# Optimization experiments

Hardware: AMD Instinct MI355X
Metric: run time of the kernel (lower is better)

Reference implementation:

```python
import math
import jax, jax.numpy as jnp
import numpy as np
from jax import lax

L = 16
T = 256
FDIM = 3
N_MIN = 4
N_MAX = 64
INIT_RANGE = 1e-4
# low 32 bits of the products are exact in uint32, and XOR + (% T) with T=256
# only reads the low 8 bits, so uint32 arithmetic matches torch's int64 exactly.
PI = jnp.array([1, 2654435761, 805459861], dtype=jnp.uint32)

def _levels():
    growth = math.exp(math.log(N_MAX / N_MIN) / (L - 1))
    return [math.floor(N_MIN * growth ** l) for l in range(L)]

def setup_inputs() -> dict:
    key = jax.random.key(0)
    kx, kt = jax.random.split(key)
    x = jax.random.uniform(kx, (4, 3, 64, 64, 64), dtype=jnp.float32)
    hash_table = (jax.random.uniform(kt, (L, T, FDIM), dtype=jnp.float32) * 2.0
                  - 1.0) * INIT_RANGE
    return {"x": x, "hash_table": hash_table}

def _forward(x, hash_table):
    b, c, h, w, d = x.shape
    outs = []
    for l, n in enumerate(_levels()):
        kh, kw, kd = h // n, w // n, d // n
        # max_pool3d with kernel==stride, VALID padding (torch default)
        pooled = lax.reduce_window(x * n, -jnp.inf, lax.max,
                                   (1, 1, kh, kw, kd), (1, 1, kh, kw, kd),
                                   'VALID')  # [b, 3, nh, nw, nd]
        g = pooled.astype(jnp.uint32)  # trunc toward zero (values >= 0)
        g = g * PI.reshape(1, 3, 1, 1, 1)
        gh = (g[:, 0] ^ g[:, 1] ^ g[:, 2]) % jnp.uint32(T)  # [b, nh, nw, nd]
        feat = hash_table[l][gh]                 # [b, nh, nw, nd, F] gather
        feat = jnp.transpose(feat, (0, 4, 1, 3, 2))  # [b, F, nh, nd, nw]
        up = jax.image.resize(feat, (b, FDIM, h, w, d), method='trilinear')
        outs.append(up)
    return jnp.concatenate(outs, axis=1)  # [b, L*F, h, w, d]

def reference(x, hash_table):
    return _forward(x, hash_table)
```

## Files before the change

kernel.cpp:

```cpp
#include <hip/hip_runtime.h>
#include <cmath>
#include <cstdint>
#include <cstddef>

using u32 = unsigned int;
typedef float f32x4 __attribute__((ext_vector_type(4)));

__device__ inline void nt_store4(float* p, float a, float b, float c, float d)
{
    f32x4 v; v.x = a; v.y = b; v.z = c; v.w = d;
    __builtin_nontemporal_store(v, (f32x4*)p);
}

constexpr int NH[12] = {4,4,5,6,8,10,12,16,21,21,32,32};

constexpr int OFF_M2  = 0;
constexpr int OFF_M3  = 393216;
constexpr int OFF_M5  = 504348;
constexpr int OFF_M4  = 525084;
constexpr int OFF_M6  = 574236;
constexpr int OFF_M8  = 586236;
constexpr int OFF_M10 = 592380;
constexpr int OFF_M12 = 594972;
constexpr int OFF_M16 = 596472;

constexpr int POFF[12] = {OFF_M16,OFF_M16,OFF_M12,OFF_M10,OFF_M8,OFF_M6,
                          OFF_M5, OFF_M4, OFF_M3, OFF_M3, OFF_M2, OFF_M2};

constexpr float invf_of(int nh){ return (float)(1.0/(64.0/(double)nh)); }
constexpr float INVF[12] = {invf_of(4),invf_of(4),invf_of(5),invf_of(6),
                            invf_of(8),invf_of(10),invf_of(12),invf_of(16),
                            invf_of(21),invf_of(21),invf_of(32),invf_of(32)};

struct HP { int n[16]; };

__device__ inline float lp(float a, float b, float w){ return fmaf(w, b - a, a); }

__global__ __launch_bounds__(256) void k_pool_base(const float* __restrict__ x,
                                                   float* __restrict__ ws)
{
    int tid = blockIdx.x * 256 + threadIdx.x;
    if (tid < 393216) {
        int pd = tid & 31, pw = (tid >> 5) & 31, ph = (tid >> 10) & 31;
        int bc = tid >> 15;
        const float* xp = x + (size_t)bc * 262144 + (ph*2)*4096 + (pw*2)*64 + pd*2;
        float2 v00 = *(const float2*)(xp);
        float2 v01 = *(const float2*)(xp + 64);
        float2 v10 = *(const float2*)(xp + 4096);
        float2 v11 = *(const float2*)(xp + 4160);
        float m = fmaxf(fmaxf(fmaxf(v00.x,v00.y), fmaxf(v01.x,v01.y)),
                        fmaxf(fmaxf(v10.x,v10.y), fmaxf(v11.x,v11.y)));
        ws[OFF_M2 + tid] = m;
    } else if (tid < 504348) {
        int idx = tid - 393216;
        int pd = idx % 21; int t2 = idx / 21;
        int pw = t2 % 21;  int t3 = t2 / 21;
        int ph = t3 % 21;  int bc = t3 / 21;
        const float* xp = x + (size_t)bc * 262144 + (ph*3)*4096 + (pw*3)*64 + pd*3;
        float m = -1.f;
        #pragma unroll
        for (int dh = 0; dh < 3; ++dh)
        #pragma unroll
        for (int dw = 0; dw < 3; ++dw) {
            const float* r = xp + dh*4096 + dw*64;
            m = fmaxf(m, fmaxf(fmaxf(r[0], r[1]), r[2]));
        }
        ws[OFF_M3 + idx] = m;
    } else if (tid < 525084) {
        int idx = tid - 504348;
        int pd = idx % 12; int t2 = idx / 12;
        int pw = t2 % 12;  int t3 = t2 / 12;
        int ph = t3 % 12;  int bc = t3 / 12;
        const float* xp = x + (size_t)bc * 262144 + (ph*5)*4096 + (pw*5)*64 + pd*5;
        float m = -1.f;
        #pragma unroll
        for (int dh = 0; dh < 5; ++dh)
        #pragma unroll
        for (int dw = 0; dw < 5; ++dw) {
            const float* r = xp + dh*4096 + dw*64;
            m = fmaxf(m, fmaxf(fmaxf(fmaxf(r[0],r[1]), fmaxf(r[2],r[3])), r[4]));
        }
        ws[OFF_M5 + idx] = m;
    }
}

__global__ __launch_bounds__(256) void k_pyr(float* __restrict__ ws)
{
    int tid = blockIdx.x * 256 + threadIdx.x;
    if (tid < 49152) {
        int w = tid >> 6, lane = tid & 63;
        int pd = w & 3, pw = (w >> 2) & 3, ph = (w >> 4) & 3, bc = w >> 6;
        const float* m2 = ws + OFF_M2 + (size_t)bc*32768 + (ph*8)*1024 + (pw*8)*32 + pd*8;
        float m = -1.f;
        #pragma unroll
        for (int e = 0; e < 8; ++e) {
            int id2 = (e << 6) | lane;
            int dd = id2 & 7, dw = (id2 >> 3) & 7, dh = id2 >> 6;
            m = fmaxf(m, m2[dh*1024 + dw*32 + dd]);
        }
        #pragma unroll
        for (int s = 32; s; s >>= 1) m = fmaxf(m, __shfl_xor(m, s, 64));
        if (lane == 0) ws[OFF_M16 + w] = m;
    } else if (tid < 98304) {
        int idx = tid - 49152;
        int pd = idx & 15, pw = (idx >> 4) & 15, ph = (idx >> 8) & 15, bc = idx >> 12;
        const float* m2 = ws + OFF_M2 + (size_t)bc*32768 + (ph*2)*1024 + (pw*2)*32 + pd*2;
        float2 u0 = *(const float2*)(m2);
        float2 u1 = *(const float2*)(m2 + 32);
        float2 u2 = *(const float2*)(m2 + 1024);
        float2 u3 = *(const float2*)(m2 + 1056);
        ws[OFF_M4 + idx] = fmaxf(fmaxf(fmaxf(u0.x,u0.y), fmaxf(u1.x,u1.y)),
                                 fmaxf(fmaxf(u2.x,u2.y), fmaxf(u3.x,u3.y)));
    } else if (tid < 110304) {
        int idx = tid - 98304;
        int pd = idx % 10; int t2 = idx / 10;
        int pw = t2 % 10;  int t3 = t2 / 10;
        int ph = t3 % 10;  int bc = t3 / 10;
        const float* m2 = ws + OFF_M2 + (size_t)bc*32768 + (ph*3)*1024 + (pw*3)*32 + pd*3;
        float m = -1.f;
        #pragma unroll
        for (int dh = 0; dh < 3; ++dh)
        #pragma unroll
        for (int dw = 0; dw < 3; ++dw) {
            const float* r = m2 + dh*1024 + dw*32;
            m = fmaxf(m, fmaxf(fmaxf(r[0], r[1]), r[2]));
        }
        ws[OFF_M6 + idx] = m;
    } else if (tid < 116448) {
        int idx = tid - 110304;
        int pd = idx & 7, pw = (idx >> 3) & 7, ph = (idx >> 6) & 7, bc = idx >> 9;
        const float* m2 = ws + OFF_M2 + (size_t)bc*32768 + (ph*4)*1024 + (pw*4)*32 + pd*4;
        float m = -1.f;
        #pragma unroll
        for (int dh = 0; dh < 4; ++dh)
        #pragma unroll
        for (int dw = 0; dw < 4; ++dw) {
            float4 v = *(const float4*)(m2 + dh*1024 + dw*32);
            m = fmaxf(m, fmaxf(fmaxf(v.x,v.y), fmaxf(v.z,v.w)));
        }
        ws[OFF_M8 + idx] = m;
    } else if (tid < 119040) {
        int idx = tid - 116448;
        int pd = idx % 6; int t2 = idx / 6;
        int pw = t2 % 6;  int t3 = t2 / 6;
        int ph = t3 % 6;  int bc = t3 / 6;
        const float* m2 = ws + OFF_M2 + (size_t)bc*32768 + (ph*5)*1024 + (pw*5)*32 + pd*5;
        float m = -1.f;
        #pragma unroll
        for (int dh = 0; dh < 5; ++dh)
        #pragma unroll
        for (int dw = 0; dw < 5; ++dw) {
            const float* r = m2 + dh*1024 + dw*32;
            m = fmaxf(m, fmaxf(fmaxf(fmaxf(r[0],r[1]), fmaxf(r[2],r[3])), r[4]));
        }
        ws[OFF_M10 + idx] = m;
    } else if (tid < 120540) {
        int idx = tid - 119040;
        int pd = idx % 5; int t2 = idx / 5;
        int pw = t2 % 5;  int t3 = t2 / 5;
        int ph = t3 % 5;  int bc = t3 / 5;
        const float* m3 = ws + OFF_M3 + (size_t)bc*9261 + (ph*4)*441 + (pw*4)*21 + pd*4;
        float m = -1.f;
        #pragma unroll
        for (int dh = 0; dh < 4; ++dh)
        #pragma unroll
        for (int dw = 0; dw < 4; ++dw) {
            const float* r = m3 + dh*441 + dw*21;
            m = fmaxf(m, fmaxf(fmaxf(r[0],r[1]), fmaxf(r[2],r[3])));
        }
        ws[OFF_M12 + idx] = m;
    }
}

__global__ __launch_bounds__(256) void k_identity(const float* __restrict__ x,
                                                  const float* __restrict__ tbl,
                                                  float* __restrict__ out, HP hp)
{
    __shared__ float  xs[3 * 2112];
    __shared__ float4 tab[1024];
    const int t = threadIdx.x;
    const int b = blockIdx.x >> 7;
    const int i = (blockIdx.x >> 1) & 63;
    const int jh = blockIdx.x & 1;

    for (int v = t; v < 1024; v += 256) {
        const float* te = tbl + (size_t)(3072 + v) * 3;
        tab[v] = make_float4(te[0], te[1], te[2], 0.f);
    }
    const float* xp = x + (size_t)b * 786432 + (size_t)i * 4096 + jh * 32;
    #pragma unroll
    for (int c = 0; c < 3; ++c)
        for (int k = t; k < 2048; k += 256) {
            int w = k >> 5, jl = k & 31;
            xs[c * 2112 + w * 33 + jl] = xp[(size_t)c * 262144 + w * 64 + jl];
        }
    __syncthreads();

    float nfs[4] = {(float)hp.n[12], (float)hp.n[13],
                    (float)hp.n[14], (float)hp.n[15]};
    float* op = out + (size_t)b * 12582912 + (size_t)36 * 262144
                    + (size_t)i * 4096 + jh * 2048;

    #pragma unroll
    for (int it = 0; it < 2; ++it) {
        int pos = it * 256 + t;
        int jl = pos >> 4, d0 = (pos & 15) << 2;
        float xv[3][4];
        #pragma unroll
        for (int dd = 0; dd < 4; ++dd) {
            int wrow = (d0 + dd) * 33 + jl;
            xv[0][dd] = xs[wrow];
            xv[1][dd] = xs[2112 + wrow];
            xv[2][dd] = xs[4224 + wrow];
        }
        #pragma unroll
        for (int u = 0; u < 4; ++u) {
            float4 f[4];
            #pragma unroll
            for (int dd = 0; dd < 4; ++dd) {
                u32 g0 = (u32)(xv[0][dd] * nfs[u]);
                u32 g1 = ((u32)(xv[1][dd] * nfs[u])) * 2654435761u;
                u32 g2 = ((u32)(xv[2][dd] * nfs[u])) * 805459861u;
                f[dd] = tab[(u << 8) | ((g0 ^ g1 ^ g2) & 255u)];
            }
            int off = u * 786432 + jl * 64 + d0;
            nt_store4(op + off,          f[0].x, f[1].x, f[2].x, f[3].x);
            nt_store4(op + off + 262144, f[0].y, f[1].y, f[2].y, f[3].y);
            nt_store4(op + off + 524288, f[0].z, f[1].z, f[2].z, f[3].z);
        }
    }
}

__global__ __launch_bounds__(256) void k_interp(const float* __restrict__ ws,
                                                const float* __restrict__ tbl,
                                                float* __restrict__ out, HP hp)
{
    __shared__ float4 plane[1056];
    const int t = threadIdx.x;
    const int l = blockIdx.y;
    const int b = blockIdx.x >> 6, i = blockIdx.x & 63;
    const int nh = NH[l];
    const int pitch = nh + 1;
    const float iv = INVF[l];
    const float nf = (float)hp.n[l];

    float fi = (float)i + 0.5f;
    float pp = fminf(fmaxf(fi * iv - 0.5f, 0.f), (float)(nh - 1));
    int p0 = min((int)pp, nh - 2);
    float wp = pp - (float)p0;

    const int nsq = nh * nh, ncb = nsq * nh;
    const float* M   = ws + POFF[l] + (size_t)b * 3 * ncb;
    const float* Mp0 = M + p0 * nsq;
    const float* Mp1 = Mp0 + nsq;
    const float* tl  = tbl + (size_t)l * 768;

    for (int idx = t; idx < nsq; idx += 256) {
        int w = idx / nh, d = idx - w * nh;
        float a0 = Mp0[idx], a1 = Mp0[idx + ncb], a2 = Mp0[idx + 2*ncb];
        u32 h0 = ((u32)(a0*nf) ^ (((u32)(a1*nf))*2654435761u)
                               ^ (((u32)(a2*nf))*805459861u)) & 255u;
        const float* t0 = tl + h0 * 3;
        float b0 = Mp1[idx], b1 = Mp1[idx + ncb], b2 = Mp1[idx + 2*ncb];
        u32 h1 = ((u32)(b0*nf) ^ (((u32)(b1*nf))*2654435761u)
                               ^ (((u32)(b2*nf))*805459861u)) & 255u;
        const float* t1 = tl + h1 * 3;
        plane[d * pitch + w] = make_float4(lp(t0[0], t1[0], wp),
                                           lp(t0[1], t1[1], wp),
                                           lp(t0[2], t1[2], wp), 0.f);
    }
    __syncthreads();

    float* op = out + (size_t)b * 12582912 + (size_t)(3 * l) * 262144 + (size_t)i * 4096;
    #pragma unroll
    for (int it = 0; it < 4; ++it) {
        int pos = it * 256 + t;
        int j = pos >> 4, d0 = (pos & 15) << 2;
        float fj = (float)j + 0.5f;
        float pr = fminf(fmaxf(fj * iv - 0.5f, 0.f), (float)(nh - 1));
        int r0 = min((int)pr, nh - 2);
        float wr = pr - (float)r0;
        const float4* P0 = plane + r0 * pitch;
        const float4* P1 = P0 + pitch;
        float ox[4], oy[4], oz[4];
        #pragma unroll
        for (int dd = 0; dd < 4; ++dd) {
            float fk = (float)(d0 + dd) + 0.5f;
            float pq = fminf(fmaxf(fk * iv - 0.5f, 0.f), (float)(nh - 1));
            int q0 = min((int)pq, nh - 2);
            float wq = pq - (float)q0;
            float4 A = P0[q0], B = P0[q0 + 1];
            float4 C = P1[q0], D = P1[q0 + 1];
            float tx = lp(A.x, B.x, wq), bx = lp(C.x, D.x, wq);
            float ty = lp(A.y, B.y, wq), by = lp(C.y, D.y, wq);
            float tz = lp(A.z, B.z, wq), bz = lp(C.z, D.z, wq);
            ox[dd] = lp(tx, bx, wr);
            oy[dd] = lp(ty, by, wr);
            oz[dd] = lp(tz, bz, wr);
        }
        int off = j * 64 + d0;
        nt_store4(op + off,          ox[0], ox[1], ox[2], ox[3]);
        nt_store4(op + off + 262144, oy[0], oy[1], oy[2], oy[3]);
        nt_store4(op + off + 524288, oz[0], oz[1], oz[2], oz[3]);
    }
}

extern "C" void kernel_launch(void* const* d_in, const int* in_sizes, int n_in,
                              void* d_out, int out_size, void* d_ws, size_t ws_size,
                              hipStream_t stream)
{
    const float* x   = (const float*)d_in[0];
    const float* tbl = (const float*)d_in[1];
    float* out = (float*)d_out;
    float* ws  = (float*)d_ws;

    HP hp;
    double growth = std::exp(std::log(16.0) / 15.0);
    for (int l = 0; l < 16; ++l)
        hp.n[l] = (int)std::floor(4.0 * std::pow(growth, (double)l));

    hipLaunchKernelGGL(k_pool_base, dim3(2052),    dim3(256), 0, stream, x, ws);
    hipLaunchKernelGGL(k_pyr,       dim3(471),     dim3(256), 0, stream, ws);
    hipLaunchKernelGGL(k_identity,  dim3(512),     dim3(256), 0, stream, x, tbl, out, hp);
    hipLaunchKernelGGL(k_interp,    dim3(256, 12), dim3(256), 0, stream, ws, tbl, out, hp);
}
```

Measured before the change: 61.33 us.

## Merge identity and interpolation kernels into one launch, use regular stores

Combines the identity-level kernel (levels 12-15) and the trilinear interpolation kernel (levels 0-11) into a single kernel launched on a 256x14 grid. Blocks branch on blockIdx.y and share one union shared-memory buffer. This removes one launch and the tail gap between the two kernels, letting both kinds of work overlap on the GPU. It also replaces nontemporal stores with plain vector stores, which changes cache behaviour for the large output write. The shared buffer grows to the larger of the two footprints, which may reduce occupancy for the interpolation blocks.

```diff
diff --git a/kernel.cpp b/kernel.cpp
--- a/kernel.cpp
+++ b/kernel.cpp
@@ -6,10 +6,10 @@
 using u32 = unsigned int;
 typedef float f32x4 __attribute__((ext_vector_type(4)));
 
-__device__ inline void nt_store4(float* p, float a, float b, float c, float d)
+__device__ inline void st4(float* p, float a, float b, float c, float d)
 {
     f32x4 v; v.x = a; v.y = b; v.z = c; v.w = d;
-    __builtin_nontemporal_store(v, (f32x4*)p);
+    *(f32x4*)p = v;
 }
 
 constexpr int NH[12] = {4,4,5,6,8,10,12,16,21,21,32,32};
@@ -172,136 +172,134 @@
     }
 }
 
-__global__ __launch_bounds__(256) void k_identity(const float* __restrict__ x,
-                                                  const float* __restrict__ tbl,
-                                                  float* __restrict__ out, HP hp)
-{
-    __shared__ float  xs[3 * 2112];
-    __shared__ float4 tab[1024];
-    const int t = threadIdx.x;
-    const int b = blockIdx.x >> 7;
-    const int i = (blockIdx.x >> 1) & 63;
-    const int jh = blockIdx.x & 1;
-
-    for (int v = t; v < 1024; v += 256) {
-        const float* te = tbl + (size_t)(3072 + v) * 3;
-        tab[v] = make_float4(te[0], te[1], te[2], 0.f);
-    }
-    const float* xp = x + (size_t)b * 786432 + (size_t)i * 4096 + jh * 32;
-    #pragma unroll
-    for (int c = 0; c < 3; ++c)
-        for (int k = t; k < 2048; k += 256) {
-            int w = k >> 5, jl = k & 31;
-            xs[c * 2112 + w * 33 + jl] = xp[(size_t)c * 262144 + w * 64 + jl];
-        }
-    __syncthreads();
-
-    float nfs[4] = {(float)hp.n[12], (float)hp.n[13],
-                    (float)hp.n[14], (float)hp.n[15]};
-    float* op = out + (size_t)b * 12582912 + (size_t)36 * 262144
-                    + (size_t)i * 4096 + jh * 2048;
-
-    #pragma unroll
-    for (int it = 0; it < 2; ++it) {
-        int pos = it * 256 + t;
-        int jl = pos >> 4, d0 = (pos & 15) << 2;
-        float xv[3][4];
-        #pragma unroll
-        for (int dd = 0; dd < 4; ++dd) {
-            int wrow = (d0 + dd) * 33 + jl;
-            xv[0][dd] = xs[wrow];
-            xv[1][dd] = xs[2112 + wrow];
-            xv[2][dd] = xs[4224 + wrow];
-        }
-        #pragma unroll
-        for (int u = 0; u < 4; ++u) {
-            float4 f[4];
-            #pragma unroll
-            for (int dd = 0; dd < 4; ++dd) {
-                u32 g0 = (u32)(xv[0][dd] * nfs[u]);
-                u32 g1 = ((u32)(xv[1][dd] * nfs[u])) * 2654435761u;
-                u32 g2 = ((u32)(xv[2][dd] * nfs[u])) * 805459861u;
-                f[dd] = tab[(u << 8) | ((g0 ^ g1 ^ g2) & 255u)];
-            }
-            int off = u * 786432 + jl * 64 + d0;
-            nt_store4(op + off,          f[0].x, f[1].x, f[2].x, f[3].x);
-            nt_store4(op + off + 262144, f[0].y, f[1].y, f[2].y, f[3].y);
-            nt_store4(op + off + 524288, f[0].z, f[1].z, f[2].z, f[3].z);
-        }
-    }
-}
-
-__global__ __launch_bounds__(256) void k_interp(const float* __restrict__ ws,
-                                                const float* __restrict__ tbl,
-                                                float* __restrict__ out, HP hp)
-{
-    __shared__ float4 plane[1056];
+__global__ __launch_bounds__(256) void k_out(const float* __restrict__ x,
+                                             const float* __restrict__ ws,
+                                             const float* __restrict__ tbl,
+                                             float* __restrict__ out, HP hp)
+{
+    __shared__ float4 shb[2608];
     const int t = threadIdx.x;
     const int l = blockIdx.y;
     const int b = blockIdx.x >> 6, i = blockIdx.x & 63;
-    const int nh = NH[l];
-    const int pitch = nh + 1;
-    const float iv = INVF[l];
-    const float nf = (float)hp.n[l];
-
-    float fi = (float)i + 0.5f;
-    float pp = fminf(fmaxf(fi * iv - 0.5f, 0.f), (float)(nh - 1));
-    int p0 = min((int)pp, nh - 2);
-    float wp = pp - (float)p0;
-
-    const int nsq = nh * nh, ncb = nsq * nh;
-    const float* M   = ws + POFF[l] + (size_t)b * 3 * ncb;
-    const float* Mp0 = M + p0 * nsq;
-    const float* Mp1 = Mp0 + nsq;
-    const float* tl  = tbl + (size_t)l * 768;
-
-    for (int idx = t; idx < nsq; idx += 256) {
-        int w = idx / nh, d = idx - w * nh;
-        float a0 = Mp0[idx], a1 = Mp0[idx + ncb], a2 = Mp0[idx + 2*ncb];
-        u32 h0 = ((u32)(a0*nf) ^ (((u32)(a1*nf))*2654435761u)
-                               ^ (((u32)(a2*nf))*805459861u)) & 255u;
-        const float* t0 = tl + h0 * 3;
-        float b0 = Mp1[idx], b1 = Mp1[idx + ncb], b2 = Mp1[idx + 2*ncb];
-        u32 h1 = ((u32)(b0*nf) ^ (((u32)(b1*nf))*2654435761u)
-                               ^ (((u32)(b2*nf))*805459861u)) & 255u;
-        const float* t1 = tl + h1 * 3;
-        plane[d * pitch + w] = make_float4(lp(t0[0], t1[0], wp),
-                                           lp(t0[1], t1[1], wp),
-                                           lp(t0[2], t1[2], wp), 0.f);
-    }
-    __syncthreads();
-
-    float* op = out + (size_t)b * 12582912 + (size_t)(3 * l) * 262144 + (size_t)i * 4096;
-    #pragma unroll
-    for (int it = 0; it < 4; ++it) {
-        int pos = it * 256 + t;
-        int j = pos >> 4, d0 = (pos & 15) << 2;
-        float fj = (float)j + 0.5f;
-        float pr = fminf(fmaxf(fj * iv - 0.5f, 0.f), (float)(nh - 1));
-        int r0 = min((int)pr, nh - 2);
-        float wr = pr - (float)r0;
-        const float4* P0 = plane + r0 * pitch;
-        const float4* P1 = P0 + pitch;
-        float ox[4], oy[4], oz[4];
-        #pragma unroll
-        for (int dd = 0; dd < 4; ++dd) {
-            float fk = (float)(d0 + dd) + 0.5f;
-            float pq = fminf(fmaxf(fk * iv - 0.5f, 0.f), (float)(nh - 1));
-            int q0 = min((int)pq, nh - 2);
-            float wq = pq - (float)q0;
-            float4 A = P0[q0], B = P0[q0 + 1];
-            float4 C = P1[q0], D = P1[q0 + 1];
-            float tx = lp(A.x, B.x, wq), bx = lp(C.x, D.x, wq);
-            float ty = lp(A.y, B.y, wq), by = lp(C.y, D.y, wq);
-            float tz = lp(A.z, B.z, wq), bz = lp(C.z, D.z, wq);
-            ox[dd] = lp(tx, bx, wr);
-            oy[dd] = lp(ty, by, wr);
-            oz[dd] = lp(tz, bz, wr);
-        }
-        int off = j * 64 + d0;
-        nt_store4(op + off,          ox[0], ox[1], ox[2], ox[3]);
-        nt_store4(op + off + 262144, oy[0], oy[1], oy[2], oy[3]);
-        nt_store4(op + off + 524288, oz[0], oz[1], oz[2], oz[3]);
+
+    if (l < 12) {
+        float4* plane = shb;
+        const int nh = NH[l];
+        const int pitch = nh + 1;
+        const float iv = INVF[l];
+        const float nf = (float)hp.n[l];
+
+        float fi = (float)i + 0.5f;
+        float pp = fminf(fmaxf(fi * iv - 0.5f, 0.f), (float)(nh - 1));
+        int p0 = min((int)pp, nh - 2);
+        float wp = pp - (float)p0;
+
+        const int nsq = nh * nh, ncb = nsq * nh;
+        const float* M   = ws + POFF[l] + (size_t)b * 3 * ncb;
+        const float* Mp0 = M + p0 * nsq;
+        const float* Mp1 = Mp0 + nsq;
+        const float* tl  = tbl + (size_t)l * 768;
+
+        for (int idx = t; idx < nsq; idx += 256) {
+            int w = idx / nh, d = idx - w * nh;
+            float a0 = Mp0[idx], a1 = Mp0[idx + ncb], a2 = Mp0[idx + 2*ncb];
+            u32 h0 = ((u32)(a0*nf) ^ (((u32)(a1*nf))*2654435761u)
+                                   ^ (((u32)(a2*nf))*805459861u)) & 255u;
+            const float* t0 = tl + h0 * 3;
+            float b0 = Mp1[idx], b1 = Mp1[idx + ncb], b2 = Mp1[idx + 2*ncb];
+            u32 h1 = ((u32)(b0*nf) ^ (((u32)(b1*nf))*2654435761u)
+                                   ^ (((u32)(b2*nf))*805459861u)) & 255u;
+            const float* t1 = tl + h1 * 3;
+            plane[d * pitch + w] = make_float4(lp(t0[0], t1[0], wp),
+                                               lp(t0[1], t1[1], wp),
+                                               lp(t0[2], t1[2], wp), 0.f);
+        }
+        __syncthreads();
+
+        float* op = out + (size_t)b * 12582912 + (size_t)(3 * l) * 262144
+                        + (size_t)i * 4096;
+        #pragma unroll
+        for (int it = 0; it < 4; ++it) {
+            int pos = it * 256 + t;
+            int j = pos >> 4, d0 = (pos & 15) << 2;
+            float fj = (float)j + 0.5f;
+            float pr = fminf(fmaxf(fj * iv - 0.5f, 0.f), (float)(nh - 1));
+            int r0 = min((int)pr, nh - 2);
+            float wr = pr - (float)r0;
+            const float4* P0 = plane + r0 * pitch;
+            const float4* P1 = P0 + pitch;
+            float ox[4], oy[4], oz[4];
+            #pragma unroll
+            for (int dd = 0; dd < 4; ++dd) {
+                float fk = (float)(d0 + dd) + 0.5f;
+                float pq = fminf(fmaxf(fk * iv - 0.5f, 0.f), (float)(nh - 1));
+                int q0 = min((int)pq, nh - 2);
+                float wq = pq - (float)q0;
+                float4 A = P0[q0], B = P0[q0 + 1];
+                float4 C = P1[q0], D = P1[q0 + 1];
+                float tx = lp(A.x, B.x, wq), bx = lp(C.x, D.x, wq);
+                float ty = lp(A.y, B.y, wq), by = lp(C.y, D.y, wq);
+                float tz = lp(A.z, B.z, wq), bz = lp(C.z, D.z, wq);
+                ox[dd] = lp(tx, bx, wr);
+                oy[dd] = lp(ty, by, wr);
+                oz[dd] = lp(tz, bz, wr);
+            }
+            int off = j * 64 + d0;
+            st4(op + off,          ox[0], ox[1], ox[2], ox[3]);
+            st4(op + off + 262144, oy[0], oy[1], oy[2], oy[3]);
+            st4(op + off + 524288, oz[0], oz[1], oz[2], oz[3]);
+        }
+    } else {
+        float4* tab = shb;
+        float*  xs  = (float*)(shb + 1024);
+        const int jh = l - 12;
+
+        for (int v = t; v < 1024; v += 256) {
+            const float* te = tbl + (size_t)(3072 + v) * 3;
+            tab[v] = make_float4(te[0], te[1], te[2], 0.f);
+        }
+        const float* xp = x + (size_t)b * 786432 + (size_t)i * 4096 + jh * 32;
+        #pragma unroll
+        for (int c = 0; c < 3; ++c)
+            for (int k = t; k < 2048; k += 256) {
+                int w = k >> 5, jl = k & 31;
+                xs[c * 2112 + w * 33 + jl] = xp[(size_t)c * 262144 + w * 64 + jl];
+            }
+        __syncthreads();
+
+        float nfs[4] = {(float)hp.n[12], (float)hp.n[13],
+                        (float)hp.n[14], (float)hp.n[15]};
+        float* op = out + (size_t)b * 12582912 + (size_t)36 * 262144
+                        + (size_t)i * 4096 + jh * 2048;
+
+        #pragma unroll
+        for (int it = 0; it < 2; ++it) {
+            int pos = it * 256 + t;
+            int jl = pos >> 4, d0 = (pos & 15) << 2;
+            float xv[3][4];
+            #pragma unroll
+            for (int dd = 0; dd < 4; ++dd) {
+                int wrow = (d0 + dd) * 33 + jl;
+                xv[0][dd] = xs[wrow];
+                xv[1][dd] = xs[2112 + wrow];
+                xv[2][dd] = xs[4224 + wrow];
+            }
+            #pragma unroll
+            for (int u = 0; u < 4; ++u) {
+                float4 f[4];
+                #pragma unroll
+                for (int dd = 0; dd < 4; ++dd) {
+                    u32 g0 = (u32)(xv[0][dd] * nfs[u]);
+                    u32 g1 = ((u32)(xv[1][dd] * nfs[u])) * 2654435761u;
+                    u32 g2 = ((u32)(xv[2][dd] * nfs[u])) * 805459861u;
+                    f[dd] = tab[(u << 8) | ((g0 ^ g1 ^ g2) & 255u)];
+                }
+                int off = u * 786432 + jl * 64 + d0;
+                st4(op + off,          f[0].x, f[1].x, f[2].x, f[3].x);
+                st4(op + off + 262144, f[0].y, f[1].y, f[2].y, f[3].y);
+                st4(op + off + 524288, f[0].z, f[1].z, f[2].z, f[3].z);
+            }
+        }
     }
 }
 
@@ -321,6 +319,5 @@
 
     hipLaunchKernelGGL(k_pool_base, dim3(2052),    dim3(256), 0, stream, x, ws);
     hipLaunchKernelGGL(k_pyr,       dim3(471),     dim3(256), 0, stream, ws);
-    hipLaunchKernelGGL(k_identity,  dim3(512),     dim3(256), 0, stream, x, tbl, out, hp);
-    hipLaunchKernelGGL(k_interp,    dim3(256, 12), dim3(256), 0, stream, ws, tbl, out, hp);
-}
+    hipLaunchKernelGGL(k_out,       dim3(256, 14), dim3(256), 0, stream, x, ws, tbl, out, hp);
+}
```

New measurement: 53.70 us. 12.5% less time.
